# Kernel tuning notes

Measured on AMD Instinct MI355X. Metric: run time of the kernel, lower is better.

The kernel has to match this reference:

```python
import jax, jax.numpy as jnp
import numpy as np

B, C, H, W = 32, 64, 32, 32
N = H * W  # 1024 spatial positions


def setup_inputs() -> dict:
    key = jax.random.key(0)
    ks = jax.random.split(key, 7)
    s_c = 1.0 / np.sqrt(C)
    s_n = 1.0 / np.sqrt(N)
    return {
        "x": jax.random.normal(ks[0], (B, C, H, W), dtype=jnp.float32),
        "w_phi": jax.random.normal(ks[1], (C, C), dtype=jnp.float32) * s_c,
        "w_theta": jax.random.normal(ks[2], (C, C), dtype=jnp.float32) * s_c,
        "w_g": jax.random.normal(ks[3], (C, C), dtype=jnp.float32) * s_c,
        "w_mask": jax.random.normal(ks[4], (C, C), dtype=jnp.float32) * s_c,
        "w_mv": jax.random.normal(ks[5], (C, C), dtype=jnp.float32) * s_c,
        "w_mk": jax.random.normal(ks[6], (N, N), dtype=jnp.float32) * s_n,
    }


def reference(x, w_phi, w_theta, w_g, w_mask, w_mv, w_mk):
    b, c, h, w = x.shape
    n = h * w
    xf = x.reshape(b, c, n)  # [b, c, N]
    # 1x1 convs == channel GEMMs (weight layout [out, in])
    phi = jnp.einsum("oc,bcn->bon", w_phi, xf)      # [b, c, N]
    theta = jnp.einsum("oc,bcn->bno", w_theta, xf)  # [b, N, c]
    g = jnp.einsum("oc,bcn->bno", w_g, xf)          # [b, N, c]
    # mv: Linear(c, c) on last dim of g  (y = g @ W^T)
    g = jnp.einsum("bnc,dc->bnd", g, w_mv)
    # theta @ phi -> [b, N, N]
    att = jnp.einsum("bnc,bcm->bnm", theta, phi)
    # mk: Linear(N, N) on last dim
    att = jnp.einsum("bnm,km->bnk", att, w_mk)
    # softmax over dim=1 (rows of the NxN map)
    att = jax.nn.softmax(att, axis=1)
    # att @ g -> [b, N, c]
    out = jnp.einsum("bnm,bmc->bnc", att, g)
    out = out.transpose(0, 2, 1).reshape(b, c, h, w)
    mask = jnp.einsum("oc,bchw->bohw", w_mask, out)
    return mask + x
```

## Files before the change

### kernel.cpp

```cpp
#include <hip/hip_runtime.h>

#define BB 32
#define CC 64
#define NN 1024

typedef __attribute__((ext_vector_type(8))) short bf8;
typedef __attribute__((ext_vector_type(4))) float f4;
typedef __attribute__((ext_vector_type(4))) unsigned short us4;

__device__ __forceinline__ unsigned short f2bf(float f) {
    unsigned u = __float_as_uint(f);
    return (unsigned short)((u + 0x7fffu + ((u >> 16) & 1u)) >> 16);
}
__device__ __forceinline__ float bf2f(unsigned short u) {
    return __uint_as_float(((unsigned)u) << 16);
}

#define MFMA(a, b, c) __builtin_amdgcn_mfma_f32_16x16x32_bf16(a, b, c, 0, 0, 0)

#define GLDS(g, l)                                                              \
    __builtin_amdgcn_global_load_lds(                                           \
        (const __attribute__((address_space(1))) void*)(g),                     \
        (__attribute__((address_space(3))) void*)(l), 16, 0, 0)

__global__ void k0_prep(const float* __restrict__ w_mv, const float* __restrict__ w_g,
                        const float* __restrict__ w_theta, const float* __restrict__ w_phi,
                        const float* __restrict__ w_mask,
                        unsigned short* __restrict__ wcat_bf,
                        unsigned short* __restrict__ wmask_bf) {
    int idx = blockIdx.x * 256 + threadIdx.x;
    int d = idx >> 6, e = idx & 63;
    float acc = 0.f;
    for (int c = 0; c < 64; ++c) acc += w_mv[d * 64 + c] * w_g[c * 64 + e];
    wcat_bf[idx] = f2bf(w_theta[idx]);
    wcat_bf[4096 + idx] = f2bf(w_phi[idx]);
    wcat_bf[8192 + idx] = f2bf(acc);
    wmask_bf[idx] = f2bf(w_mask[idx]);
}

__global__ void k0b_wmk(const float* __restrict__ wmk, unsigned short* __restrict__ wmk_bf) {
    int i = (blockIdx.x * 256 + threadIdx.x) * 4;
    float4 v = *(const float4*)(wmk + i);
    us4 r;
    r.x = f2bf(v.x); r.y = f2bf(v.y); r.z = f2bf(v.z); r.w = f2bf(v.w);
    *(us4*)(wmk_bf + i) = r;
}

__global__ __launch_bounds__(256, 4) void k1_channel(const float* __restrict__ x,
                                                     const unsigned short* __restrict__ wcat,
                                                     unsigned short* __restrict__ theta_nc,
                                                     unsigned short* __restrict__ phi_cm,
                                                     unsigned short* __restrict__ g2_cm) {
    __shared__ unsigned short xT[64][66];
    int b = blockIdx.y;
    int n0 = blockIdx.x * 64;
    int tid = threadIdx.x;
    int w = tid >> 6, lane = tid & 63, l16 = lane & 15, q = lane >> 4;
    size_t bo = (size_t)b * CC * NN;
#pragma unroll
    for (int i = 0; i < 16; ++i) {
        int idx = i * 256 + tid;
        int c = idx >> 6, n2 = idx & 63;
        xT[n2][c] = f2bf(x[bo + (size_t)c * NN + n0 + n2]);
    }
    __syncthreads();
    bf8 bF[4][2];
#pragma unroll
    for (int ct = 0; ct < 4; ++ct) {
        bF[ct][0] = *(const bf8*)&xT[ct * 16 + l16][q * 8];
        bF[ct][1] = *(const bf8*)&xT[ct * 16 + l16][32 + q * 8];
    }
#pragma unroll
    for (int rt = 0; rt < 3; ++rt) {
        int R = w * 48 + rt * 16;
        const unsigned short* wa = wcat + (R + l16) * 64 + q * 8;
        bf8 a0 = *(const bf8*)wa;
        bf8 a1 = *(const bf8*)(wa + 32);
        int which = R >> 6, rb = R & 63;
#pragma unroll
        for (int ct = 0; ct < 4; ++ct) {
            f4 acc = {0.f, 0.f, 0.f, 0.f};
            acc = MFMA(a0, bF[ct][0], acc);
            acc = MFMA(a1, bF[ct][1], acc);
            int n = n0 + ct * 16 + l16;
            if (which == 0) {
                us4 t;
                t.x = f2bf(acc[0]); t.y = f2bf(acc[1]);
                t.z = f2bf(acc[2]); t.w = f2bf(acc[3]);
                *(us4*)&theta_nc[bo + (size_t)n * 64 + rb + q * 4] = t;
            } else {
                unsigned short* dst = (which == 1 ? phi_cm : g2_cm) + bo;
#pragma unroll
                for (int r = 0; r < 4; ++r)
                    dst[(size_t)(rb + q * 4 + r) * NN + n] = f2bf(acc[r]);
            }
        }
    }
}

__global__ __launch_bounds__(512, 4) void k2_phi2(const unsigned short* __restrict__ phi_cm,
                                                  const unsigned short* __restrict__ wmk_bf,
                                                  unsigned short* __restrict__ phi2t) {
    __shared__ unsigned short bT[2][4096];
    __shared__ float red[64][68];
    int b = blockIdx.y;
    int k0 = blockIdx.x * 64;
    int tid = threadIdx.x;
    int w = tid >> 6, lane = tid & 63, l16 = lane & 15, q = lane >> 4;
    int e8 = lane >> 3, c8 = (lane & 7) * 8;
    int ks = w & 3, mh = w >> 2;
    size_t bo = (size_t)b * CC * NN;
    const unsigned short* phib = phi_cm + bo;
    const unsigned short* arow = wmk_bf + (size_t)(k0 + ks * 16 + l16) * NN + q * 8;
    f4 acc[4];
#pragma unroll
    for (int tc = 0; tc < 4; ++tc) acc[tc] = (f4){0.f, 0.f, 0.f, 0.f};

#pragma unroll 1
    for (int mc = 0; mc < 8; ++mc) {
        int m0 = mh * 512 + mc * 64;
        bf8 a0 = *(const bf8*)(arow + m0);
        bf8 a1 = *(const bf8*)(arow + m0 + 32);
        __syncthreads();
        const unsigned short* gg = phib + (size_t)(ks * 16 + e8) * NN + m0 + c8;
        GLDS(gg, &bT[mh][ks * 1024]);
        GLDS(gg + (size_t)8 * NN, &bT[mh][ks * 1024 + 512]);
        __syncthreads();
#pragma unroll
        for (int tc = 0; tc < 4; ++tc) {
            bf8 b0 = *(const bf8*)&bT[mh][(tc * 16 + l16) * 64 + q * 8];
            bf8 b1 = *(const bf8*)&bT[mh][(tc * 16 + l16) * 64 + 32 + q * 8];
            acc[tc] = MFMA(a0, b0, acc[tc]);
            acc[tc] = MFMA(a1, b1, acc[tc]);
        }
    }
    __syncthreads();
    if (mh == 1) {
#pragma unroll
        for (int tc = 0; tc < 4; ++tc)
#pragma unroll
            for (int r = 0; r < 4; ++r) red[ks * 16 + q * 4 + r][tc * 16 + l16] = acc[tc][r];
    }
    __syncthreads();
    if (mh == 0) {
        unsigned short* prow = phi2t + bo;
#pragma unroll
        for (int tc = 0; tc < 4; ++tc)
#pragma unroll
            for (int r = 0; r < 4; ++r) {
                float v = acc[tc][r] + red[ks * 16 + q * 4 + r][tc * 16 + l16];
                prow[(size_t)(k0 + ks * 16 + q * 4 + r) * 64 + tc * 16 + l16] = f2bf(v);
            }
    }
}

__global__ __launch_bounds__(512, 4) void k3_stats(const unsigned short* __restrict__ theta_nc,
                                                   const unsigned short* __restrict__ phi2t,
                                                   const unsigned short* __restrict__ g2_cm,
                                                   unsigned short* __restrict__ g3_cm) {
    __shared__ float sred[8][64];
    __shared__ float svs[64];
    int b = blockIdx.y;
    int k0 = blockIdx.x * 64;
    int tid = threadIdx.x;
    int w = tid >> 6, lane = tid & 63, l16 = lane & 15, q = lane >> 4;
    int wq = w & 3, nh = w >> 2;
    size_t bo = (size_t)b * CC * NN;
    bf8 bF[4][2];
#pragma unroll
    for (int tc = 0; tc < 4; ++tc)
#pragma unroll
        for (int kc = 0; kc < 2; ++kc)
            bF[tc][kc] = *(const bf8*)(phi2t + bo + (size_t)(k0 + tc * 16 + l16) * 64 + kc * 32 + q * 8);
    float s[4] = {0.f, 0.f, 0.f, 0.f};
    const unsigned short* thb = theta_nc + bo + q * 8;
    int nbase = nh * 8;
    int nrow0 = (nbase + 0) * 64 + wq * 16 + l16;
    bf8 a0 = *(const bf8*)(thb + (size_t)nrow0 * 64);
    bf8 a1 = *(const bf8*)(thb + (size_t)nrow0 * 64 + 32);
    for (int nb = 0; nb < 8; ++nb) {
        bf8 p0, p1;
        if (nb < 7) {
            int nr = (nbase + nb + 1) * 64 + wq * 16 + l16;
            p0 = *(const bf8*)(thb + (size_t)nr * 64);
            p1 = *(const bf8*)(thb + (size_t)nr * 64 + 32);
        }
#pragma unroll
        for (int tc = 0; tc < 4; ++tc) {
            f4 acc = {0.f, 0.f, 0.f, 0.f};
            acc = MFMA(a0, bF[tc][0], acc);
            acc = MFMA(a1, bF[tc][1], acc);
            s[tc] += __expf(acc[0]) + __expf(acc[1]) + __expf(acc[2]) + __expf(acc[3]);
        }
        a0 = p0;
        a1 = p1;
    }
#pragma unroll
    for (int tc = 0; tc < 4; ++tc) {
        s[tc] += __shfl_xor(s[tc], 16, 64);
        s[tc] += __shfl_xor(s[tc], 32, 64);
    }
    if (q == 0) {
#pragma unroll
        for (int tc = 0; tc < 4; ++tc) sred[w][tc * 16 + l16] = s[tc];
    }
    __syncthreads();
    if (tid < 64) {
        float S = 0.f;
#pragma unroll
        for (int ww = 0; ww < 8; ++ww) S += sred[ww][tid];
        svs[tid] = 1.f / S;
    }
    __syncthreads();
    int c0 = tid >> 6, kl = tid & 63;
#pragma unroll
    for (int i = 0; i < 8; ++i) {
        int c = c0 * 8 + i;
        size_t ix = bo + (size_t)c * NN + k0 + kl;
        g3_cm[ix] = f2bf(bf2f(g2_cm[ix]) * svs[kl]);
    }
}

__global__ __launch_bounds__(512, 4) void k4_out(const unsigned short* __restrict__ theta_nc,
                                                 const unsigned short* __restrict__ phi2t,
                                                 const unsigned short* __restrict__ g3_cm,
                                                 const unsigned short* __restrict__ wmask_bf,
                                                 const float* __restrict__ x,
                                                 float* __restrict__ out) {
    __shared__ unsigned short stage[16384];
    __shared__ unsigned short P_lds[2][64][72];
    __shared__ unsigned short o_lds[64][72];
    int b = blockIdx.y;
    int n0 = blockIdx.x * 64;
    int tid = threadIdx.x;
    int w = tid >> 6, lane = tid & 63, l16 = lane & 15, q = lane >> 4;
    int e8 = lane >> 3, c8 = (lane & 7) * 8;
    int ws = w & 3, mh = w >> 2;
    int nl = ws * 16 + l16;
    size_t bo = (size_t)b * CC * NN;
    unsigned short* aT = stage + mh * 4096;
    unsigned short* gT = stage + 8192 + mh * 4096;
    bf8 thB[2];
#pragma unroll
    for (int kc = 0; kc < 2; ++kc)
        thB[kc] = *(const bf8*)(theta_nc + bo + (size_t)(n0 + nl) * 64 + kc * 32 + q * 8);
    f4 accO[4];
#pragma unroll
    for (int tr = 0; tr < 4; ++tr) accO[tr] = (f4){0.f, 0.f, 0.f, 0.f};
    const unsigned short* p2b = phi2t + bo;
    const unsigned short* g3b = g3_cm + bo;

#pragma unroll 1
    for (int mc = 0; mc < 8; ++mc) {
        int m0 = mh * 512 + mc * 64;
        __syncthreads();
        {
            int r = ws * 16 + e8;
            const unsigned short* ga = p2b + (size_t)(m0 + r) * 64 + c8;
            GLDS(ga, aT + ws * 1024);
            GLDS(ga + 8 * 64, aT + ws * 1024 + 512);
            const unsigned short* gg = g3b + (size_t)r * NN + m0 + c8;
            GLDS(gg, gT + ws * 1024);
            GLDS(gg + (size_t)8 * NN, gT + ws * 1024 + 512);
        }
        __syncthreads();
#pragma unroll
        for (int tr = 0; tr < 4; ++tr) {
            int row = (tr * 16 + l16) * 64;
            bf8 a0 = *(const bf8*)&aT[row + q * 8];
            bf8 a1 = *(const bf8*)&aT[row + 32 + q * 8];
            f4 at = {0.f, 0.f, 0.f, 0.f};
            at = MFMA(a0, thB[0], at);
            at = MFMA(a1, thB[1], at);
            us4 pk;
            pk.x = f2bf(__expf(at[0]));
            pk.y = f2bf(__expf(at[1]));
            pk.z = f2bf(__expf(at[2]));
            pk.w = f2bf(__expf(at[3]));
            *(us4*)&P_lds[mh][nl][tr * 16 + q * 4] = pk;
        }
        bf8 pF0 = *(const bf8*)&P_lds[mh][nl][q * 8];
        bf8 pF1 = *(const bf8*)&P_lds[mh][nl][32 + q * 8];
#pragma unroll
        for (int tr = 0; tr < 4; ++tr) {
            int row = (tr * 16 + l16) * 64;
            bf8 g0 = *(const bf8*)&gT[row + q * 8];
            bf8 g1 = *(const bf8*)&gT[row + 32 + q * 8];
            accO[tr] = MFMA(g0, pF0, accO[tr]);
            accO[tr] = MFMA(g1, pF1, accO[tr]);
        }
    }
    __syncthreads();
    float (*o_red)[68] = (float(*)[68])(void*)stage;
    if (mh == 1) {
#pragma unroll
        for (int tr = 0; tr < 4; ++tr)
#pragma unroll
            for (int r = 0; r < 4; ++r) o_red[tr * 16 + q * 4 + r][nl] = accO[tr][r];
    }
    __syncthreads();
    if (mh == 0) {
#pragma unroll
        for (int tr = 0; tr < 4; ++tr) {
            us4 ov;
            ov.x = f2bf(accO[tr][0] + o_red[tr * 16 + q * 4 + 0][nl]);
            ov.y = f2bf(accO[tr][1] + o_red[tr * 16 + q * 4 + 1][nl]);
            ov.z = f2bf(accO[tr][2] + o_red[tr * 16 + q * 4 + 2][nl]);
            ov.w = f2bf(accO[tr][3] + o_red[tr * 16 + q * 4 + 3][nl]);
            *(us4*)&o_lds[nl][tr * 16 + q * 4] = ov;
        }
    }
    __syncthreads();
    bf8 oB0 = *(const bf8*)&o_lds[nl][q * 8];
    bf8 oB1 = *(const bf8*)&o_lds[nl][32 + q * 8];
#pragma unroll
    for (int t2 = 0; t2 < 2; ++t2) {
        int tr = mh * 2 + t2;
        const unsigned short* wa = wmask_bf + (tr * 16 + l16) * 64 + q * 8;
        bf8 w0 = *(const bf8*)wa;
        bf8 w1 = *(const bf8*)(wa + 32);
        f4 accF = {0.f, 0.f, 0.f, 0.f};
        accF = MFMA(w0, oB0, accF);
        accF = MFMA(w1, oB1, accF);
#pragma unroll
        for (int r = 0; r < 4; ++r) {
            size_t ix = bo + (size_t)(tr * 16 + q * 4 + r) * NN + n0 + nl;
            out[ix] = accF[r] + x[ix];
        }
    }
}

extern "C" void kernel_launch(void* const* d_in, const int* in_sizes, int n_in,
                              void* d_out, int out_size, void* d_ws, size_t ws_size,
                              hipStream_t stream) {
    const float* x       = (const float*)d_in[0];
    const float* w_phi   = (const float*)d_in[1];
    const float* w_theta = (const float*)d_in[2];
    const float* w_g     = (const float*)d_in[3];
    const float* w_mask  = (const float*)d_in[4];
    const float* w_mv    = (const float*)d_in[5];
    const float* w_mk    = (const float*)d_in[6];
    float* out = (float*)d_out;

    const size_t CN = (size_t)BB * CC * NN;
    char* p = (char*)d_ws;
    unsigned short* theta_nc = (unsigned short*)p; p += CN * 2;
    unsigned short* phi_cm = (unsigned short*)p;   p += CN * 2;
    unsigned short* g2_cm = (unsigned short*)p;    p += CN * 2;
    unsigned short* g3_cm = (unsigned short*)p;    p += CN * 2;
    unsigned short* phi2t = (unsigned short*)p;    p += CN * 2;
    unsigned short* wmk_bf = (unsigned short*)p;   p += (size_t)NN * NN * 2;
    unsigned short* wcat_bf = (unsigned short*)p;  p += 192 * 64 * 2;
    unsigned short* wmask_bf = (unsigned short*)p; p += 4096 * 2;

    k0_prep<<<16, 256, 0, stream>>>(w_mv, w_g, w_theta, w_phi, w_mask, wcat_bf, wmask_bf);
    k0b_wmk<<<1024, 256, 0, stream>>>(w_mk, wmk_bf);
    k1_channel<<<dim3(16, BB), 256, 0, stream>>>(x, wcat_bf, theta_nc, phi_cm, g2_cm);
    k2_phi2<<<dim3(16, BB), 512, 0, stream>>>(phi_cm, wmk_bf, phi2t);
    k3_stats<<<dim3(16, BB), 512, 0, stream>>>(theta_nc, phi2t, g2_cm, g3_cm);
    k4_out<<<dim3(16, BB), 512, 0, stream>>>(theta_nc, phi2t, g3_cm, wmask_bf, x, out);
}
```

Measured before the change: 139.6 us.

## Replace LDS staging with direct global loads in GEMM kernels; merge prep launches

In k2_phi2 and k4_out, the MFMA operands are now read straight from global memory into registers instead of being staged through shared memory with global_load_lds. This removes the two block-wide barriers per loop iteration, and the loops are unrolled by 2 so loads can overlap compute. The cost is that waves sharing an operand tile each fetch it separately, so they rely on L1/L2 cache hits instead of a single shared LDS copy. The two weight-preparation kernels are also merged into one launch to save launch overhead.

```diff
diff --git a/kernel.cpp b/kernel.cpp
--- a/kernel.cpp
+++ b/kernel.cpp
@@ -18,32 +18,29 @@
 
 #define MFMA(a, b, c) __builtin_amdgcn_mfma_f32_16x16x32_bf16(a, b, c, 0, 0, 0)
 
-#define GLDS(g, l)                                                              \
-    __builtin_amdgcn_global_load_lds(                                           \
-        (const __attribute__((address_space(1))) void*)(g),                     \
-        (__attribute__((address_space(3))) void*)(l), 16, 0, 0)
-
 __global__ void k0_prep(const float* __restrict__ w_mv, const float* __restrict__ w_g,
                         const float* __restrict__ w_theta, const float* __restrict__ w_phi,
-                        const float* __restrict__ w_mask,
+                        const float* __restrict__ w_mask, const float* __restrict__ w_mk,
                         unsigned short* __restrict__ wcat_bf,
-                        unsigned short* __restrict__ wmask_bf) {
-    int idx = blockIdx.x * 256 + threadIdx.x;
-    int d = idx >> 6, e = idx & 63;
-    float acc = 0.f;
-    for (int c = 0; c < 64; ++c) acc += w_mv[d * 64 + c] * w_g[c * 64 + e];
-    wcat_bf[idx] = f2bf(w_theta[idx]);
-    wcat_bf[4096 + idx] = f2bf(w_phi[idx]);
-    wcat_bf[8192 + idx] = f2bf(acc);
-    wmask_bf[idx] = f2bf(w_mask[idx]);
-}
-
-__global__ void k0b_wmk(const float* __restrict__ wmk, unsigned short* __restrict__ wmk_bf) {
-    int i = (blockIdx.x * 256 + threadIdx.x) * 4;
-    float4 v = *(const float4*)(wmk + i);
-    us4 r;
-    r.x = f2bf(v.x); r.y = f2bf(v.y); r.z = f2bf(v.z); r.w = f2bf(v.w);
-    *(us4*)(wmk_bf + i) = r;
+                        unsigned short* __restrict__ wmask_bf,
+                        unsigned short* __restrict__ wmk_bf) {
+    int tid = threadIdx.x;
+    if (blockIdx.x < 1024) {
+        int i = (blockIdx.x * 256 + tid) * 4;
+        float4 v = *(const float4*)(w_mk + i);
+        us4 r;
+        r.x = f2bf(v.x); r.y = f2bf(v.y); r.z = f2bf(v.z); r.w = f2bf(v.w);
+        *(us4*)(wmk_bf + i) = r;
+    } else {
+        int idx = (blockIdx.x - 1024) * 256 + tid;
+        int d = idx >> 6, e = idx & 63;
+        float acc = 0.f;
+        for (int c = 0; c < 64; ++c) acc += w_mv[d * 64 + c] * w_g[c * 64 + e];
+        wcat_bf[idx] = f2bf(w_theta[idx]);
+        wcat_bf[4096 + idx] = f2bf(w_phi[idx]);
+        wcat_bf[8192 + idx] = f2bf(acc);
+        wmask_bf[idx] = f2bf(w_mask[idx]);
+    }
 }
 
 __global__ __launch_bounds__(256, 4) void k1_channel(const float* __restrict__ x,
@@ -101,40 +98,33 @@
 __global__ __launch_bounds__(512, 4) void k2_phi2(const unsigned short* __restrict__ phi_cm,
                                                   const unsigned short* __restrict__ wmk_bf,
                                                   unsigned short* __restrict__ phi2t) {
-    __shared__ unsigned short bT[2][4096];
     __shared__ float red[64][68];
     int b = blockIdx.y;
     int k0 = blockIdx.x * 64;
     int tid = threadIdx.x;
     int w = tid >> 6, lane = tid & 63, l16 = lane & 15, q = lane >> 4;
-    int e8 = lane >> 3, c8 = (lane & 7) * 8;
     int ks = w & 3, mh = w >> 2;
     size_t bo = (size_t)b * CC * NN;
-    const unsigned short* phib = phi_cm + bo;
+    const unsigned short* phib = phi_cm + bo + q * 8;
     const unsigned short* arow = wmk_bf + (size_t)(k0 + ks * 16 + l16) * NN + q * 8;
     f4 acc[4];
 #pragma unroll
     for (int tc = 0; tc < 4; ++tc) acc[tc] = (f4){0.f, 0.f, 0.f, 0.f};
 
-#pragma unroll 1
+#pragma unroll 2
     for (int mc = 0; mc < 8; ++mc) {
         int m0 = mh * 512 + mc * 64;
         bf8 a0 = *(const bf8*)(arow + m0);
         bf8 a1 = *(const bf8*)(arow + m0 + 32);
-        __syncthreads();
-        const unsigned short* gg = phib + (size_t)(ks * 16 + e8) * NN + m0 + c8;
-        GLDS(gg, &bT[mh][ks * 1024]);
-        GLDS(gg + (size_t)8 * NN, &bT[mh][ks * 1024 + 512]);
-        __syncthreads();
 #pragma unroll
         for (int tc = 0; tc < 4; ++tc) {
-            bf8 b0 = *(const bf8*)&bT[mh][(tc * 16 + l16) * 64 + q * 8];
-            bf8 b1 = *(const bf8*)&bT[mh][(tc * 16 + l16) * 64 + 32 + q * 8];
+            const unsigned short* bp = phib + (size_t)(tc * 16 + l16) * NN + m0;
+            bf8 b0 = *(const bf8*)bp;
+            bf8 b1 = *(const bf8*)(bp + 32);
             acc[tc] = MFMA(a0, b0, acc[tc]);
             acc[tc] = MFMA(a1, b1, acc[tc]);
         }
     }
-    __syncthreads();
     if (mh == 1) {
 #pragma unroll
         for (int tc = 0; tc < 4; ++tc)
@@ -227,19 +217,16 @@
                                                  const unsigned short* __restrict__ wmask_bf,
                                                  const float* __restrict__ x,
                                                  float* __restrict__ out) {
-    __shared__ unsigned short stage[16384];
     __shared__ unsigned short P_lds[2][64][72];
+    __shared__ float o_red[64][68];
     __shared__ unsigned short o_lds[64][72];
     int b = blockIdx.y;
     int n0 = blockIdx.x * 64;
     int tid = threadIdx.x;
     int w = tid >> 6, lane = tid & 63, l16 = lane & 15, q = lane >> 4;
-    int e8 = lane >> 3, c8 = (lane & 7) * 8;
     int ws = w & 3, mh = w >> 2;
     int nl = ws * 16 + l16;
     size_t bo = (size_t)b * CC * NN;
-    unsigned short* aT = stage + mh * 4096;
-    unsigned short* gT = stage + 8192 + mh * 4096;
     bf8 thB[2];
 #pragma unroll
     for (int kc = 0; kc < 2; ++kc)
@@ -247,28 +234,17 @@
     f4 accO[4];
 #pragma unroll
     for (int tr = 0; tr < 4; ++tr) accO[tr] = (f4){0.f, 0.f, 0.f, 0.f};
-    const unsigned short* p2b = phi2t + bo;
-    const unsigned short* g3b = g3_cm + bo;
-
-#pragma unroll 1
+    const unsigned short* p2b = phi2t + bo + q * 8;
+    const unsigned short* g3b = g3_cm + bo + q * 8;
+
+#pragma unroll 2
     for (int mc = 0; mc < 8; ++mc) {
         int m0 = mh * 512 + mc * 64;
-        __syncthreads();
-        {
-            int r = ws * 16 + e8;
-            const unsigned short* ga = p2b + (size_t)(m0 + r) * 64 + c8;
-            GLDS(ga, aT + ws * 1024);
-            GLDS(ga + 8 * 64, aT + ws * 1024 + 512);
-            const unsigned short* gg = g3b + (size_t)r * NN + m0 + c8;
-            GLDS(gg, gT + ws * 1024);
-            GLDS(gg + (size_t)8 * NN, gT + ws * 1024 + 512);
-        }
-        __syncthreads();
 #pragma unroll
         for (int tr = 0; tr < 4; ++tr) {
-            int row = (tr * 16 + l16) * 64;
-            bf8 a0 = *(const bf8*)&aT[row + q * 8];
-            bf8 a1 = *(const bf8*)&aT[row + 32 + q * 8];
+            const unsigned short* ap = p2b + (size_t)(m0 + tr * 16 + l16) * 64;
+            bf8 a0 = *(const bf8*)ap;
+            bf8 a1 = *(const bf8*)(ap + 32);
             f4 at = {0.f, 0.f, 0.f, 0.f};
             at = MFMA(a0, thB[0], at);
             at = MFMA(a1, thB[1], at);
@@ -283,15 +259,13 @@
         bf8 pF1 = *(const bf8*)&P_lds[mh][nl][32 + q * 8];
 #pragma unroll
         for (int tr = 0; tr < 4; ++tr) {
-            int row = (tr * 16 + l16) * 64;
-            bf8 g0 = *(const bf8*)&gT[row + q * 8];
-            bf8 g1 = *(const bf8*)&gT[row + 32 + q * 8];
+            const unsigned short* gp = g3b + (size_t)(tr * 16 + l16) * NN + m0;
+            bf8 g0 = *(const bf8*)gp;
+            bf8 g1 = *(const bf8*)(gp + 32);
             accO[tr] = MFMA(g0, pF0, accO[tr]);
             accO[tr] = MFMA(g1, pF1, accO[tr]);
         }
     }
-    __syncthreads();
-    float (*o_red)[68] = (float(*)[68])(void*)stage;
     if (mh == 1) {
 #pragma unroll
         for (int tr = 0; tr < 4; ++tr)
@@ -353,8 +327,8 @@
     unsigned short* wcat_bf = (unsigned short*)p;  p += 192 * 64 * 2;
     unsigned short* wmask_bf = (unsigned short*)p; p += 4096 * 2;
 
-    k0_prep<<<16, 256, 0, stream>>>(w_mv, w_g, w_theta, w_phi, w_mask, wcat_bf, wmask_bf);
-    k0b_wmk<<<1024, 256, 0, stream>>>(w_mk, wmk_bf);
+    k0_prep<<<1040, 256, 0, stream>>>(w_mv, w_g, w_theta, w_phi, w_mask, w_mk,
+                                      wcat_bf, wmask_bf, wmk_bf);
     k1_channel<<<dim3(16, BB), 256, 0, stream>>>(x, wcat_bf, theta_nc, phi_cm, g2_cm);
     k2_phi2<<<dim3(16, BB), 512, 0, stream>>>(phi_cm, wmk_bf, phi2t);
     k3_stats<<<dim3(16, BB), 512, 0, stream>>>(theta_nc, phi2t, g2_cm, g3_cm);
```

After: 194.6 us. 1.39x slower.
